# Kernel tuning notes

Hardware: AMD Instinct MI355X
Metric: run time of the kernel (lower is better)

Reference implementation:

```python
import jax, jax.numpy as jnp
import numpy as np

VOCAB, EMB, HID = 27, 32, 64
B, T = 4096, 256

def setup_inputs() -> dict:
    key = jax.random.key(0)
    ks = jax.random.split(key, 7)
    return {
        "X": jax.random.randint(ks[0], (B, T), 0, VOCAB),
        "emb_w": jax.random.normal(ks[1], (VOCAB, EMB), jnp.float32),
        "start": jax.random.normal(ks[2], (1, HID), jnp.float32),
        "rnn_w": jax.random.normal(ks[3], (HID, EMB + HID), jnp.float32) * 0.1,
        "rnn_b": jax.random.normal(ks[4], (HID,), jnp.float32) * 0.1,
        "lm_w": jax.random.normal(ks[5], (VOCAB, HID), jnp.float32) * 0.1,
        "lm_b": jax.random.normal(ks[6], (VOCAB,), jnp.float32) * 0.1,
    }

def reference(X, emb_w, start, rnn_w, rnn_b, lm_w, lm_b):
    emb = emb_w[X]                      # [B, T, EMB]
    h0 = jnp.broadcast_to(start, (X.shape[0], HID))  # [B, HID]
    # split rnn weight: concat(emb, h) @ W^T == emb @ Wx^T + h @ Wh^T
    Wx = rnn_w[:, :EMB]                 # [HID, EMB]
    Wh = rnn_w[:, EMB:]                 # [HID, HID]
    emb_t = jnp.swapaxes(emb, 0, 1)     # [T, B, EMB]
    # precompute input projections (batched, no sequential dep)
    xproj = jnp.einsum('tbe,he->tbh', emb_t, Wx) + rnn_b  # [T, B, HID]

    def step(h, xp):
        h_new = jnp.tanh(xp + h @ Wh.T)
        return h_new, h_new

    _, hiddens = jax.lax.scan(step, h0, xproj)  # [T, B, HID]
    hiddens = jnp.swapaxes(hiddens, 0, 1)        # [B, T, HID]
    logits = jnp.einsum('bth,vh->btv', hiddens, lm_w) + lm_b  # [B, T, VOCAB]
    return logits
```

## Files before the change

kernel.cpp:

```cpp
#include <hip/hip_runtime.h>

#define VOCAB 27
#define EMB   32
#define HID   64
#define BATCH 4096
#define TLEN  256
#define ROWS  16
#define WROW  96
#define TPAD  65
#define HROW  72

typedef __attribute__((ext_vector_type(8))) short bf16x8;
typedef __attribute__((ext_vector_type(4))) float f32x4;

__device__ __forceinline__ float fast_tanh(float x) {
    float t = __builtin_amdgcn_exp2f(x * 2.885390081777927f);
    float r = __builtin_amdgcn_rcpf(t + 1.0f);
    return fmaf(-2.0f, r, 1.0f);
}
__device__ __forceinline__ unsigned bfbits(float f) {
    return (__float_as_uint(f) + 0x8000u) >> 16;
}

union Frag { unsigned u[4]; bf16x8 v; };

__device__ __forceinline__ f32x4 mfma16(bf16x8 a, bf16x8 b, f32x4 c) {
    return __builtin_amdgcn_mfma_f32_16x16x32_bf16(a, b, c, 0, 0, 0);
}

__global__ __launch_bounds__(256, 1) void rnn_mfma4(
    const int*   __restrict__ X,
    const float* __restrict__ emb_w,
    const float* __restrict__ start,
    const float* __restrict__ rnn_w,
    const float* __restrict__ rnn_b,
    const float* __restrict__ lm_w,
    const float* __restrict__ lm_b,
    float*       __restrict__ out)
{
    __shared__ __align__(16) float          tabf[VOCAB * TPAD];
    __shared__ __align__(16) unsigned short Hhi[2][ROWS * HROW];
    __shared__ __align__(16) unsigned short Hlo[2][ROWS * HROW];
    __shared__               unsigned char  tok8[ROWS * TLEN];

    const int tid  = threadIdx.x;
    const int lane = tid & 63;
    const int w    = tid >> 6;
    const int cc   = lane & 15;
    const int q    = lane >> 4;
    const int b0   = blockIdx.x * ROWS;
    const int colh = w * 16 + cc;

    for (int f = tid; f < VOCAB * HID; f += 256) {
        const int v = f >> 6, i = f & 63;
        float s = rnn_b[i];
        #pragma unroll
        for (int e = 0; e < EMB; ++e)
            s = fmaf(rnn_w[i * WROW + e], emb_w[v * EMB + e], s);
        tabf[v * TPAD + i] = s;
    }
    for (int idx = tid; idx < ROWS * TLEN; idx += 256) {
        const int r = idx >> 8, t = idx & 255;
        tok8[idx] = (unsigned char)X[(size_t)(b0 + r) * TLEN + t];
    }
    for (int idx = tid; idx < ROWS * HID; idx += 256) {
        const int r = idx >> 6, j = idx & 63;
        const float s = start[j];
        const unsigned hb = bfbits(s);
        Hhi[1][r * HROW + j] = (unsigned short)hb;
        Hlo[1][r * HROW + j] = (unsigned short)bfbits(s - __uint_as_float(hb << 16));
    }

    Frag whh[2], whl[2];
    #pragma unroll
    for (int kc = 0; kc < 2; ++kc) {
        const float* wr = &rnn_w[colh * WROW + EMB + q * 8 + kc * 32];
        #pragma unroll
        for (int p = 0; p < 4; ++p) {
            const float w0 = wr[2 * p], w1 = wr[2 * p + 1];
            const unsigned h0 = bfbits(w0), h1 = bfbits(w1);
            whh[kc].u[p] = h0 | (h1 << 16);
            whl[kc].u[p] = bfbits(w0 - __uint_as_float(h0 << 16)) |
                           (bfbits(w1 - __uint_as_float(h1 << 16)) << 16);
        }
    }
    Frag lwh[2], lwl[2];
    float lb = 0.0f;
    if (w >= 2) {
        const int  nt = w - 2;
        const int  v  = nt * 16 + cc;
        const bool ok = v < VOCAB;
        #pragma unroll
        for (int kc = 0; kc < 2; ++kc) {
            const float* wr = &lm_w[(ok ? v : 0) * HID + q * 8 + kc * 32];
            #pragma unroll
            for (int p = 0; p < 4; ++p) {
                const float w0 = ok ? wr[2 * p] : 0.0f;
                const float w1 = ok ? wr[2 * p + 1] : 0.0f;
                const unsigned h0 = bfbits(w0), h1 = bfbits(w1);
                lwh[kc].u[p] = h0 | (h1 << 16);
                lwl[kc].u[p] = bfbits(w0 - __uint_as_float(h0 << 16)) |
                               (bfbits(w1 - __uint_as_float(h1 << 16)) << 16);
            }
        }
        lb = ok ? lm_b[v] : 0.0f;
    }

    __syncthreads();

    Frag ah[2], al[2];
    #pragma unroll
    for (int kc = 0; kc < 2; ++kc) {
        ah[kc].v = *(const bf16x8*)&Hhi[1][cc * HROW + q * 8 + kc * 32];
        al[kc].v = *(const bf16x8*)&Hlo[1][cc * HROW + q * 8 + kc * 32];
    }
    int   tkn[4];
    float xq[4];
    #pragma unroll
    for (int r = 0; r < 4; ++r) {
        tkn[r] = tok8[(4 * q + r) * TLEN];
        xq[r]  = tabf[tkn[r] * TPAD + colh];
    }

    for (int t = 0; t < TLEN; ++t) {
        const int tn = (t + 1) & (TLEN - 1);
        #pragma unroll
        for (int r = 0; r < 4; ++r)
            tkn[r] = tok8[(4 * q + r) * TLEN + tn];

        f32x4 a0 = {xq[0], xq[1], xq[2], xq[3]};
        f32x4 a1 = {0.0f, 0.0f, 0.0f, 0.0f};
        f32x4 a2 = {0.0f, 0.0f, 0.0f, 0.0f};
        a0 = mfma16(ah[0].v, whh[0].v, a0); a0 = mfma16(ah[1].v, whh[1].v, a0);
        a1 = mfma16(al[0].v, whh[0].v, a1); a1 = mfma16(al[1].v, whh[1].v, a1);
        a2 = mfma16(ah[0].v, whl[0].v, a2); a2 = mfma16(ah[1].v, whl[1].v, a2);

        const int buf = t & 1;
        #pragma unroll
        for (int r = 0; r < 4; ++r) {
            const float hv = fast_tanh((a0[r] + a1[r]) + a2[r]);
            const unsigned hb = bfbits(hv);
            Hhi[buf][(4 * q + r) * HROW + colh] = (unsigned short)hb;
            Hlo[buf][(4 * q + r) * HROW + colh] =
                (unsigned short)bfbits(hv - __uint_as_float(hb << 16));
        }

        __syncthreads();

        #pragma unroll
        for (int kc = 0; kc < 2; ++kc) {
            ah[kc].v = *(const bf16x8*)&Hhi[buf][cc * HROW + q * 8 + kc * 32];
            al[kc].v = *(const bf16x8*)&Hlo[buf][cc * HROW + q * 8 + kc * 32];
        }
        #pragma unroll
        for (int r = 0; r < 4; ++r)
            xq[r] = tabf[tkn[r] * TPAD + colh];

        if (w >= 2) {
            f32x4 g0 = {lb, lb, lb, lb};
            f32x4 g1 = {0.0f, 0.0f, 0.0f, 0.0f};
            f32x4 g2 = {0.0f, 0.0f, 0.0f, 0.0f};
            g0 = mfma16(ah[0].v, lwh[0].v, g0); g0 = mfma16(ah[1].v, lwh[1].v, g0);
            g1 = mfma16(al[0].v, lwh[0].v, g1); g1 = mfma16(al[1].v, lwh[1].v, g1);
            g2 = mfma16(ah[0].v, lwl[0].v, g2); g2 = mfma16(ah[1].v, lwl[1].v, g2);
            const int col = (w - 2) * 16 + cc;
            if (col < VOCAB) {
                const size_t base =
                    ((size_t)(b0 + 4 * q) * TLEN + t) * VOCAB + col;
                #pragma unroll
                for (int r = 0; r < 4; ++r)
                    out[base + (size_t)r * (TLEN * VOCAB)] = (g0[r] + g1[r]) + g2[r];
            }
        }
    }
}

extern "C" void kernel_launch(void* const* d_in, const int* in_sizes, int n_in,
                              void* d_out, int out_size, void* d_ws, size_t ws_size,
                              hipStream_t stream) {
    const int*   X     = (const int*)  d_in[0];
    const float* emb_w = (const float*)d_in[1];
    const float* start = (const float*)d_in[2];
    const float* rnn_w = (const float*)d_in[3];
    const float* rnn_b = (const float*)d_in[4];
    const float* lm_w  = (const float*)d_in[5];
    const float* lm_b  = (const float*)d_in[6];
    float*       out   = (float*)d_out;

    dim3 grid(BATCH / ROWS);
    dim3 block(256);
    rnn_mfma4<<<grid, block, 0, stream>>>(X, emb_w, start, rnn_w, rnn_b,
                                          lm_w, lm_b, out);
}
```

Baseline: 244.3 us.

## Halve batch rows per block and overlap LM-head MFMA with the step barrier

Each block now handles 8 batch rows inside a 16-row MFMA tile, with the other rows padded to zero, so the grid doubles to 512 blocks. Launch bounds no longer force one block per CU, so more blocks can share a CU. The LM-head projection for the previous step's hidden state now runs before the barrier, overlapping the recurrence, and a lighter LDS-only barrier replaces __syncthreads. The trade is that half of every MFMA is spent on padding rows, and a tail step is added to emit the last logits.

```diff
diff --git a/kernel.cpp b/kernel.cpp
--- a/kernel.cpp
+++ b/kernel.cpp
@@ -5,7 +5,8 @@
 #define HID   64
 #define BATCH 4096
 #define TLEN  256
-#define ROWS  16
+#define ROWS  8
+#define TILE  16
 #define WROW  96
 #define TPAD  65
 #define HROW  72
@@ -28,7 +29,14 @@
     return __builtin_amdgcn_mfma_f32_16x16x32_bf16(a, b, c, 0, 0, 0);
 }
 
-__global__ __launch_bounds__(256, 1) void rnn_mfma4(
+__device__ __forceinline__ void lds_barrier() {
+    asm volatile("s_waitcnt lgkmcnt(0)" : : : "memory");
+    __builtin_amdgcn_sched_barrier(0);
+    __builtin_amdgcn_s_barrier();
+    __builtin_amdgcn_sched_barrier(0);
+}
+
+__global__ __launch_bounds__(256) void rnn_mfma8(
     const int*   __restrict__ X,
     const float* __restrict__ emb_w,
     const float* __restrict__ start,
@@ -39,9 +47,9 @@
     float*       __restrict__ out)
 {
     __shared__ __align__(16) float          tabf[VOCAB * TPAD];
-    __shared__ __align__(16) unsigned short Hhi[2][ROWS * HROW];
-    __shared__ __align__(16) unsigned short Hlo[2][ROWS * HROW];
-    __shared__               unsigned char  tok8[ROWS * TLEN];
+    __shared__ __align__(16) unsigned short Hhi[2][TILE * HROW];
+    __shared__ __align__(16) unsigned short Hlo[2][TILE * HROW];
+    __shared__               unsigned char  tok8[TILE * TLEN];
 
     const int tid  = threadIdx.x;
     const int lane = tid & 63;
@@ -59,11 +67,12 @@
             s = fmaf(rnn_w[i * WROW + e], emb_w[v * EMB + e], s);
         tabf[v * TPAD + i] = s;
     }
-    for (int idx = tid; idx < ROWS * TLEN; idx += 256) {
+    for (int idx = tid; idx < TILE * TLEN; idx += 256) {
         const int r = idx >> 8, t = idx & 255;
-        tok8[idx] = (unsigned char)X[(size_t)(b0 + r) * TLEN + t];
-    }
-    for (int idx = tid; idx < ROWS * HID; idx += 256) {
+        tok8[idx] = (r < ROWS)
+            ? (unsigned char)X[(size_t)(b0 + r) * TLEN + t] : (unsigned char)0;
+    }
+    for (int idx = tid; idx < TILE * HID; idx += 256) {
         const int r = idx >> 6, j = idx & 63;
         const float s = start[j];
         const unsigned hb = bfbits(s);
@@ -87,8 +96,7 @@
     Frag lwh[2], lwl[2];
     float lb = 0.0f;
     if (w >= 2) {
-        const int  nt = w - 2;
-        const int  v  = nt * 16 + cc;
+        const int  v  = (w - 2) * 16 + cc;
         const bool ok = v < VOCAB;
         #pragma unroll
         for (int kc = 0; kc < 2; ++kc) {
@@ -145,7 +153,17 @@
                 (unsigned short)bfbits(hv - __uint_as_float(hb << 16));
         }
 
-        __syncthreads();
+        f32x4 g0 = {0.0f, 0.0f, 0.0f, 0.0f};
+        f32x4 g1 = {0.0f, 0.0f, 0.0f, 0.0f};
+        f32x4 g2 = {0.0f, 0.0f, 0.0f, 0.0f};
+        if (w >= 2 && t > 0) {
+            g0 = (f32x4){lb, lb, lb, lb};
+            g0 = mfma16(ah[0].v, lwh[0].v, g0); g0 = mfma16(ah[1].v, lwh[1].v, g0);
+            g1 = mfma16(al[0].v, lwh[0].v, g1); g1 = mfma16(al[1].v, lwh[1].v, g1);
+            g2 = mfma16(ah[0].v, lwl[0].v, g2); g2 = mfma16(ah[1].v, lwl[1].v, g2);
+        }
+
+        lds_barrier();
 
         #pragma unroll
         for (int kc = 0; kc < 2; ++kc) {
@@ -156,21 +174,36 @@
         for (int r = 0; r < 4; ++r)
             xq[r] = tabf[tkn[r] * TPAD + colh];
 
-        if (w >= 2) {
-            f32x4 g0 = {lb, lb, lb, lb};
-            f32x4 g1 = {0.0f, 0.0f, 0.0f, 0.0f};
-            f32x4 g2 = {0.0f, 0.0f, 0.0f, 0.0f};
-            g0 = mfma16(ah[0].v, lwh[0].v, g0); g0 = mfma16(ah[1].v, lwh[1].v, g0);
-            g1 = mfma16(al[0].v, lwh[0].v, g1); g1 = mfma16(al[1].v, lwh[1].v, g1);
-            g2 = mfma16(ah[0].v, lwl[0].v, g2); g2 = mfma16(ah[1].v, lwl[1].v, g2);
+        if (w >= 2 && t > 0) {
             const int col = (w - 2) * 16 + cc;
             if (col < VOCAB) {
                 const size_t base =
-                    ((size_t)(b0 + 4 * q) * TLEN + t) * VOCAB + col;
+                    ((size_t)(b0 + 4 * q) * TLEN + (t - 1)) * VOCAB + col;
                 #pragma unroll
                 for (int r = 0; r < 4; ++r)
-                    out[base + (size_t)r * (TLEN * VOCAB)] = (g0[r] + g1[r]) + g2[r];
+                    if (4 * q + r < ROWS)
+                        out[base + (size_t)r * (TLEN * VOCAB)] =
+                            (g0[r] + g1[r]) + g2[r];
             }
+        }
+    }
+
+    if (w >= 2) {
+        f32x4 g0 = {lb, lb, lb, lb};
+        f32x4 g1 = {0.0f, 0.0f, 0.0f, 0.0f};
+        f32x4 g2 = {0.0f, 0.0f, 0.0f, 0.0f};
+        g0 = mfma16(ah[0].v, lwh[0].v, g0); g0 = mfma16(ah[1].v, lwh[1].v, g0);
+        g1 = mfma16(al[0].v, lwh[0].v, g1); g1 = mfma16(al[1].v, lwh[1].v, g1);
+        g2 = mfma16(ah[0].v, lwl[0].v, g2); g2 = mfma16(ah[1].v, lwl[1].v, g2);
+        const int col = (w - 2) * 16 + cc;
+        if (col < VOCAB) {
+            const size_t base =
+                ((size_t)(b0 + 4 * q) * TLEN + (TLEN - 1)) * VOCAB + col;
+            #pragma unroll
+            for (int r = 0; r < 4; ++r)
+                if (4 * q + r < ROWS)
+                    out[base + (size_t)r * (TLEN * VOCAB)] =
+                        (g0[r] + g1[r]) + g2[r];
         }
     }
 }
@@ -189,6 +222,6 @@
 
     dim3 grid(BATCH / ROWS);
     dim3 block(256);
-    rnn_mfma4<<<grid, block, 0, stream>>>(X, emb_w, start, rnn_w, rnn_b,
+    rnn_mfma8<<<grid, block, 0, stream>>>(X, emb_w, start, rnn_w, rnn_b,
                                           lm_w, lm_b, out);
 }
```

Result: slower. 299.6 us (+22.6%).
